# Kernel optimization log

Measured on AMD Instinct MI355X. Metric: run time of the kernel, lower is better.

The kernel has to match this reference:

```python
import jax, jax.numpy as jnp
import numpy as np

N, E, B = 50000, 300000, 8
XD, ED, H, L, G = 160, 16, 256, 4, 32


def setup_inputs() -> dict:
    key = jax.random.key(0)
    ks = jax.random.split(key, 24)
    w = lambda k, shape: jax.random.normal(k, shape, jnp.float32) * 0.05
    z = lambda *shape: jnp.zeros(shape, jnp.float32)
    in_dim = G + (XD - 128)
    return {
        "x": jax.random.normal(ks[0], (N, XD), jnp.float32),
        "edge_attr": jax.random.normal(ks[1], (E, ED), jnp.float32),
        "geo_w": w(ks[2], (128, G)), "geo_b": z(G),
        "nin_w1": w(ks[3], (in_dim, H)), "nin_b1": z(H),
        "nin_w2": w(ks[4], (H, H)), "nin_b2": z(H),
        "ee_w1": w(ks[5], (ED, H)), "ee_b1": z(H),
        "ee_w2": w(ks[6], (H, H)), "ee_b2": z(H),
        "msgx_w": w(ks[7], (L, H, H)),
        "msge_w": w(ks[8], (L, H, H)),
        "upd_w1": w(ks[9], (L, H, H)), "upd_b1": z(L, H),
        "upd_w2": w(ks[10], (L, H, H)), "upd_b2": z(L, H),
        "ln_g": jnp.ones((L, H), jnp.float32), "ln_b": z(L, H),
        "edge_index": jax.random.randint(ks[11], (2, E), 0, N),
        "batch": jnp.sort(jax.random.randint(ks[12], (N,), 0, B)),
        "node_type": jax.random.randint(ks[13], (N,), 0, 3),
    }


def _layernorm(v, g, b, eps=1e-5):
    mu = v.mean(-1, keepdims=True)
    var = ((v - mu) ** 2).mean(-1, keepdims=True)
    return (v - mu) / jnp.sqrt(var + eps) * g + b


def reference(x, edge_attr, geo_w, geo_b, nin_w1, nin_b1, nin_w2, nin_b2,
              ee_w1, ee_b1, ee_w2, ee_b2, msgx_w, msge_w,
              upd_w1, upd_b1, upd_w2, upd_b2, ln_g, ln_b,
              edge_index, batch, node_type):
    # geo projection of leading 128 dims, concat with remaining features
    geo = jax.nn.relu(x[:, :128] @ geo_w + geo_b)
    xin = jnp.concatenate([geo, x[:, 128:]], axis=1)
    # node_in MLP
    h = jax.nn.relu(xin @ nin_w1 + nin_b1) @ nin_w2 + nin_b2  # [N, H]
    # edge encoder MLP
    e = jax.nn.relu(edge_attr @ ee_w1 + ee_b1) @ ee_w2 + ee_b2  # [E, H]
    src, dst = edge_index[0], edge_index[1]
    for l in range(L):
        # message: msg_x(x_j) + msg_e(e), scatter-add to target nodes
        m = h[src] @ msgx_w[l] + e @ msge_w[l]  # [E, H]
        agg = jax.ops.segment_sum(m, dst, num_segments=N)  # [N, H]
        u = jax.nn.relu(agg @ upd_w1[l] + upd_b1[l]) @ upd_w2[l] + upd_b2[l]
        h = _layernorm(h + u, ln_g[l], ln_b[l])
    # masked mean-pool per graph for each node type
    def pool(k):
        mask = (node_type == k).astype(h.dtype)[:, None]  # [N, 1]
        s = jax.ops.segment_sum(h * mask, batch, num_segments=B)
        c = jax.ops.segment_sum(mask, batch, num_segments=B)
        return s / jnp.maximum(c, 1.0)
    z = jnp.concatenate([pool(0), pool(1), pool(2)], axis=1)  # [B, 3H]
    return (z, h, batch)
```

## Files before the change

kernel.cpp:

```cpp
#include <hip/hip_runtime.h>

constexpr int N  = 50000;
constexpr int E  = 300000;
constexpr int B  = 8;
constexpr int XD = 160;
constexpr int ED = 16;
constexpr int H  = 256;
constexpr int L  = 4;
constexpr int G  = 32;

typedef __attribute__((ext_vector_type(8))) short short8;
typedef __attribute__((ext_vector_type(4))) short sv4;
typedef __attribute__((ext_vector_type(4))) float floatx4;

__device__ __forceinline__ short f2bf(float f) {
    union { float f; unsigned u; } v; v.f = f;
    unsigned r = (v.u + 0x7fffu + ((v.u >> 16) & 1u)) >> 16;
    return (short)r;
}
__device__ __forceinline__ float bf2f(short s) {
    union { unsigned u; float f; } v;
    v.u = ((unsigned)(unsigned short)s) << 16;
    return v.f;
}

__global__ __launch_bounds__(256) void hist_kernel(
    const int* __restrict__ dst, int* __restrict__ cnt)
{
    int e = blockIdx.x * 256 + threadIdx.x;
    if (e < E) atomicAdd(&cnt[dst[e]], 1);
}

__global__ __launch_bounds__(256) void scan_partial_kernel(
    const int* __restrict__ cnt, int* __restrict__ bsum)
{
    __shared__ int s[256];
    const int tid = threadIdx.x;
    int i = blockIdx.x * 256 + tid;
    s[tid] = (i < N) ? cnt[i] : 0;
    __syncthreads();
    #pragma unroll
    for (int off = 128; off > 0; off >>= 1) {
        if (tid < off) s[tid] += s[tid + off];
        __syncthreads();
    }
    if (tid == 0) bsum[blockIdx.x] = s[0];
}

__global__ __launch_bounds__(256) void scan_bsum_kernel(
    int* __restrict__ bsum, int nb, int* __restrict__ rsN)
{
    __shared__ int s[256];
    const int tid = threadIdx.x;
    int v = (tid < nb) ? bsum[tid] : 0;
    s[tid] = v;
    __syncthreads();
    #pragma unroll
    for (int off = 1; off < 256; off <<= 1) {
        int x = (tid >= off) ? s[tid - off] : 0;
        __syncthreads();
        s[tid] += x;
        __syncthreads();
    }
    if (tid < nb) bsum[tid] = s[tid] - v;
    if (tid == 255) *rsN = s[255];
}

__global__ __launch_bounds__(256) void scan_final_kernel(
    const int* __restrict__ cnt, const int* __restrict__ bsum,
    int* __restrict__ rs, int* __restrict__ cursor)
{
    __shared__ int s[256];
    const int tid = threadIdx.x;
    int i = blockIdx.x * 256 + tid;
    int v = (i < N) ? cnt[i] : 0;
    s[tid] = v;
    __syncthreads();
    #pragma unroll
    for (int off = 1; off < 256; off <<= 1) {
        int x = (tid >= off) ? s[tid - off] : 0;
        __syncthreads();
        s[tid] += x;
        __syncthreads();
    }
    int excl = s[tid] - v + bsum[blockIdx.x];
    if (i < N) { rs[i] = excl; cursor[i] = excl; }
}

__global__ __launch_bounds__(256) void fill_kernel(
    const int* __restrict__ src, const int* __restrict__ dst,
    const float* __restrict__ ea,
    int* __restrict__ cursor, int* __restrict__ csr_src,
    float* __restrict__ ea_csr)
{
    int e = blockIdx.x * 256 + threadIdx.x;
    if (e < E) {
        int d = dst[e];
        int pos = atomicAdd(&cursor[d], 1);
        csr_src[pos] = src[e];
        const float4* a = (const float4*)(ea + (size_t)e * ED);
        float4* o = (float4*)(ea_csr + (size_t)pos * ED);
        o[0] = a[0]; o[1] = a[1]; o[2] = a[2]; o[3] = a[3];
    }
}

__global__ __launch_bounds__(256) void hidden_agg_kernel(
    const float* __restrict__ ea_csr, const float* __restrict__ ew1,
    const float* __restrict__ eb1,
    const int* __restrict__ rs,
    short* __restrict__ haggB)
{
    const int lane = threadIdx.x & 63;
    const int wave = threadIdx.x >> 6;
    const int n = blockIdx.x * 4 + wave;
    if (n >= N) return;

    float4 w[ED];
    #pragma unroll
    for (int k = 0; k < ED; ++k)
        w[k] = *(const float4*)&ew1[k * H + 4 * lane];
    float4 bb = *(const float4*)&eb1[4 * lane];

    const int s = rs[n], e = rs[n + 1];
    float4 acc = {0.f, 0.f, 0.f, 0.f};
    int j = s;
    for (; j + 1 < e; j += 2) {
        const float4* r0 = (const float4*)(ea_csr + (size_t)j * ED);
        const float4* r1 = (const float4*)(ea_csr + (size_t)(j + 1) * ED);
        float4 p0[4] = {r0[0], r0[1], r0[2], r0[3]};
        float4 p1[4] = {r1[0], r1[1], r1[2], r1[3]};
        float4 h0 = bb, h1 = bb;
        #pragma unroll
        for (int q = 0; q < 4; ++q) {
            float v00 = p0[q].x, v01 = p0[q].y, v02 = p0[q].z, v03 = p0[q].w;
            float v10 = p1[q].x, v11 = p1[q].y, v12 = p1[q].z, v13 = p1[q].w;
            const float4 w0 = w[q * 4 + 0], w1 = w[q * 4 + 1];
            const float4 w2 = w[q * 4 + 2], w3 = w[q * 4 + 3];
            h0.x += v00 * w0.x + v01 * w1.x + v02 * w2.x + v03 * w3.x;
            h0.y += v00 * w0.y + v01 * w1.y + v02 * w2.y + v03 * w3.y;
            h0.z += v00 * w0.z + v01 * w1.z + v02 * w2.z + v03 * w3.z;
            h0.w += v00 * w0.w + v01 * w1.w + v02 * w2.w + v03 * w3.w;
            h1.x += v10 * w0.x + v11 * w1.x + v12 * w2.x + v13 * w3.x;
            h1.y += v10 * w0.y + v11 * w1.y + v12 * w2.y + v13 * w3.y;
            h1.z += v10 * w0.z + v11 * w1.z + v12 * w2.z + v13 * w3.z;
            h1.w += v10 * w0.w + v11 * w1.w + v12 * w2.w + v13 * w3.w;
        }
        acc.x += fmaxf(h0.x, 0.f) + fmaxf(h1.x, 0.f);
        acc.y += fmaxf(h0.y, 0.f) + fmaxf(h1.y, 0.f);
        acc.z += fmaxf(h0.z, 0.f) + fmaxf(h1.z, 0.f);
        acc.w += fmaxf(h0.w, 0.f) + fmaxf(h1.w, 0.f);
    }
    if (j < e) {
        const float4* r0 = (const float4*)(ea_csr + (size_t)j * ED);
        float4 p0[4] = {r0[0], r0[1], r0[2], r0[3]};
        float4 h0 = bb;
        #pragma unroll
        for (int q = 0; q < 4; ++q) {
            float v00 = p0[q].x, v01 = p0[q].y, v02 = p0[q].z, v03 = p0[q].w;
            const float4 w0 = w[q * 4 + 0], w1 = w[q * 4 + 1];
            const float4 w2 = w[q * 4 + 2], w3 = w[q * 4 + 3];
            h0.x += v00 * w0.x + v01 * w1.x + v02 * w2.x + v03 * w3.x;
            h0.y += v00 * w0.y + v01 * w1.y + v02 * w2.y + v03 * w3.y;
            h0.z += v00 * w0.z + v01 * w1.z + v02 * w2.z + v03 * w3.z;
            h0.w += v00 * w0.w + v01 * w1.w + v02 * w2.w + v03 * w3.w;
        }
        acc.x += fmaxf(h0.x, 0.f); acc.y += fmaxf(h0.y, 0.f);
        acc.z += fmaxf(h0.z, 0.f); acc.w += fmaxf(h0.w, 0.f);
    }
    sv4 o = {f2bf(acc.x), f2bf(acc.y), f2bf(acc.z), f2bf(acc.w)};
    *(sv4*)&haggB[(size_t)n * H + 4 * lane] = o;
}

__global__ __launch_bounds__(256) void gather_kernel(
    const short* __restrict__ h_in_bf,
    const int* __restrict__ rs, const int* __restrict__ csr_src,
    short* __restrict__ agg_bf)
{
    const int lane = threadIdx.x & 63;
    const int wave = threadIdx.x >> 6;
    const int n = blockIdx.x * 4 + wave;
    if (n >= N) return;
    const int s = rs[n], e = rs[n + 1];
    float4 acc = {0.f, 0.f, 0.f, 0.f};
    int j = s;
    for (; j + 4 <= e; j += 4) {
        const int s0 = csr_src[j],     s1 = csr_src[j + 1];
        const int s2 = csr_src[j + 2], s3 = csr_src[j + 3];
        sv4 v0 = *(const sv4*)&h_in_bf[(size_t)s0 * H + 4 * lane];
        sv4 v1 = *(const sv4*)&h_in_bf[(size_t)s1 * H + 4 * lane];
        sv4 v2 = *(const sv4*)&h_in_bf[(size_t)s2 * H + 4 * lane];
        sv4 v3 = *(const sv4*)&h_in_bf[(size_t)s3 * H + 4 * lane];
        acc.x += (bf2f(v0.x) + bf2f(v1.x)) + (bf2f(v2.x) + bf2f(v3.x));
        acc.y += (bf2f(v0.y) + bf2f(v1.y)) + (bf2f(v2.y) + bf2f(v3.y));
        acc.z += (bf2f(v0.z) + bf2f(v1.z)) + (bf2f(v2.z) + bf2f(v3.z));
        acc.w += (bf2f(v0.w) + bf2f(v1.w)) + (bf2f(v2.w) + bf2f(v3.w));
    }
    for (; j < e; ++j) {
        const int s0 = csr_src[j];
        sv4 v0 = *(const sv4*)&h_in_bf[(size_t)s0 * H + 4 * lane];
        acc.x += bf2f(v0.x); acc.y += bf2f(v0.y);
        acc.z += bf2f(v0.z); acc.w += bf2f(v0.w);
    }
    sv4 o = {f2bf(acc.x), f2bf(acc.y), f2bf(acc.z), f2bf(acc.w)};
    *(sv4*)&agg_bf[(size_t)n * H + 4 * lane] = o;
}

__global__ __launch_bounds__(256) void we_fuse_kernel(
    const float* __restrict__ ee_w2, const float* __restrict__ msge_w,
    float* __restrict__ WEf32)
{
    __shared__ float wrow[H];
    const int tid = threadIdx.x;
    const int l = blockIdx.x / H;
    const int t = blockIdx.x % H;
    wrow[tid] = ee_w2[t * H + tid];
    __syncthreads();
    const float* mw = msge_w + (size_t)l * H * H;
    float acc = 0.f;
    for (int k = 0; k < H; ++k)
        acc += wrow[k] * mw[k * H + tid];
    WEf32[((size_t)l * H + t) * H + tid] = acc;
}

__global__ __launch_bounds__(256) void fuse1_kernel(
    const float* __restrict__ msgx_w, const float* __restrict__ upd_w1,
    short* __restrict__ fusedT)
{
    __shared__ float wrow[H];
    const int tid = threadIdx.x;
    const int l = blockIdx.x / H;
    const int t = blockIdx.x % H;
    wrow[tid] = msgx_w[((size_t)l * H + t) * H + tid];
    __syncthreads();
    const float* w1 = upd_w1 + (size_t)l * H * H;
    float acc = 0.f;
    for (int j = 0; j < H; ++j)
        acc += wrow[j] * w1[j * H + tid];
    fusedT[((size_t)(l * H + tid)) * 512 + t] = f2bf(acc);
}

__global__ __launch_bounds__(256) void fuse2_kernel(
    const float* __restrict__ WEf32, const float* __restrict__ upd_w1,
    short* __restrict__ fusedT)
{
    __shared__ float wrow[H];
    const int tid = threadIdx.x;
    const int l = blockIdx.x / H;
    const int t = blockIdx.x % H;
    wrow[tid] = WEf32[((size_t)l * H + t) * H + tid];
    __syncthreads();
    const float* w1 = upd_w1 + (size_t)l * H * H;
    float acc = 0.f;
    for (int j = 0; j < H; ++j)
        acc += wrow[j] * w1[j * H + tid];
    fusedT[((size_t)(l * H + tid)) * 512 + 256 + t] = f2bf(acc);
}

__global__ __launch_bounds__(256) void fuse_b_kernel(
    const float* __restrict__ ee_b2, const float* __restrict__ msge_w,
    float* __restrict__ be2)
{
    __shared__ float brow[H];
    const int tid = threadIdx.x;
    const int l = blockIdx.x;
    brow[tid] = ee_b2[tid];
    __syncthreads();
    const float* mw = msge_w + (size_t)l * H * H;
    float acc = 0.f;
    for (int k = 0; k < H; ++k)
        acc += brow[k] * mw[k * H + tid];
    be2[l * H + tid] = acc;
}

__global__ __launch_bounds__(256) void fuse_bias_kernel(
    const float* __restrict__ be2, const float* __restrict__ upd_w1,
    float* __restrict__ be2w1)
{
    __shared__ float brow[H];
    const int tid = threadIdx.x;
    const int l = blockIdx.x;
    brow[tid] = be2[l * H + tid];
    __syncthreads();
    const float* w1 = upd_w1 + (size_t)l * H * H;
    float acc = 0.f;
    for (int j = 0; j < H; ++j)
        acc += brow[j] * w1[j * H + tid];
    be2w1[l * H + tid] = acc;
}

__global__ __launch_bounds__(256) void conv_bt_kernel(
    const float* __restrict__ w, short* __restrict__ bt)
{
    int mat = blockIdx.x >> 8, k = blockIdx.x & 255, n = threadIdx.x;
    bt[((size_t)mat * H + n) * H + k] = f2bf(w[((size_t)mat * H + k) * H + n]);
}

__global__ __launch_bounds__(256) void geow_bt_kernel(
    const float* __restrict__ w, short* __restrict__ bt)
{
    for (int i = threadIdx.x; i < 32 * 128; i += 256) {
        int n = i >> 7, k = i & 127;
        bt[i] = f2bf(w[k * 32 + n]);
    }
}

__global__ __launch_bounds__(256) void ninw1_bt_kernel(
    const float* __restrict__ w, short* __restrict__ bt)
{
    int i = blockIdx.x * 256 + threadIdx.x;
    int n = i >> 6, k = i & 63;
    bt[i] = f2bf(w[k * H + n]);
}

__global__ __launch_bounds__(256) void node_in_mfma_kernel(
    const float* __restrict__ x,
    const short* __restrict__ geo_wbt, const float* __restrict__ geo_b,
    const short* __restrict__ w1bt, const float* __restrict__ b1,
    const short* __restrict__ w2bt, const float* __restrict__ b2,
    short* __restrict__ h_bf)
{
    constexpr int KP = H + 8;
    constexpr int KX = 128 + 8;
    constexpr int KI = 64 + 8;
    __shared__ short A[64 * KP];
    __shared__ short XIN[64 * KI];
    const int tid = threadIdx.x;
    const int lane = tid & 63, wave = tid >> 6;
    const int quad = lane >> 4, lm = lane & 15;
    const int n0 = blockIdx.x * 64;
    const int nvalid = min(64, N - n0);
    const int ncol = wave * 64 + lm;

    for (int i = tid; i < 64 * 128; i += 256) {
        int row = i >> 7, k = i & 127;
        float v = (row < nvalid) ? x[(size_t)(n0 + row) * XD + k] : 0.f;
        A[row * KX + k] = f2bf(v);
    }
    for (int i = tid; i < 64 * 32; i += 256) {
        int row = i >> 5, k = i & 31;
        float v = (row < nvalid) ? x[(size_t)(n0 + row) * XD + 128 + k] : 0.f;
        XIN[row * KI + 32 + k] = f2bf(v);
    }
    __syncthreads();

    {
        floatx4 c[2];
        float b0 = geo_b[lm], b1v = geo_b[16 + lm];
        c[0] = {b0, b0, b0, b0};
        c[1] = {b1v, b1v, b1v, b1v};
        #pragma unroll
        for (int ks = 0; ks < 4; ++ks) {
            short8 a  = *(const short8*)&A[(wave * 16 + lm) * KX + ks * 32 + quad * 8];
            short8 w0 = *(const short8*)&geo_wbt[(size_t)lm * 128 + ks * 32 + quad * 8];
            short8 w1 = *(const short8*)&geo_wbt[(size_t)(16 + lm) * 128 + ks * 32 + quad * 8];
            c[0] = __builtin_amdgcn_mfma_f32_16x16x32_bf16(a, w0, c[0], 0, 0, 0);
            c[1] = __builtin_amdgcn_mfma_f32_16x16x32_bf16(a, w1, c[1], 0, 0, 0);
        }
        #pragma unroll
        for (int nt = 0; nt < 2; ++nt)
            #pragma unroll
            for (int r = 0; r < 4; ++r) {
                int row = wave * 16 + quad * 4 + r;
                XIN[row * KI + nt * 16 + lm] = f2bf(fmaxf(c[nt][r], 0.f));
            }
    }
    __syncthreads();

    floatx4 c1[4][4];
    #pragma unroll
    for (int nt = 0; nt < 4; ++nt) {
        float bb = b1[ncol + nt * 16];
        #pragma unroll
        for (int mt = 0; mt < 4; ++mt) {
            c1[mt][nt][0] = bb; c1[mt][nt][1] = bb;
            c1[mt][nt][2] = bb; c1[mt][nt][3] = bb;
        }
    }
    #pragma unroll
    for (int ks = 0; ks < 2; ++ks) {
        short8 a[4], b[4];
        #pragma unroll
        for (int mt = 0; mt < 4; ++mt)
            a[mt] = *(const short8*)&XIN[(mt * 16 + lm) * KI + ks * 32 + quad * 8];
        #pragma unroll
        for (int nt = 0; nt < 4; ++nt)
            b[nt] = *(const short8*)&w1bt[(size_t)(ncol + nt * 16) * 64 + ks * 32 + quad * 8];
        #pragma unroll
        for (int mt = 0; mt < 4; ++mt)
            #pragma unroll
            for (int nt = 0; nt < 4; ++nt)
                c1[mt][nt] = __builtin_amdgcn_mfma_f32_16x16x32_bf16(a[mt], b[nt], c1[mt][nt], 0, 0, 0);
    }
    __syncthreads();
    #pragma unroll
    for (int mt = 0; mt < 4; ++mt)
        #pragma unroll
        for (int nt = 0; nt < 4; ++nt) {
            int col = ncol + nt * 16;
            #pragma unroll
            for (int r = 0; r < 4; ++r) {
                int row = mt * 16 + quad * 4 + r;
                A[row * KP + col] = f2bf(fmaxf(c1[mt][nt][r], 0.f));
            }
        }
    __syncthreads();

    floatx4 c2[4][4];
    #pragma unroll
    for (int nt = 0; nt < 4; ++nt) {
        float bb = b2[ncol + nt * 16];
        #pragma unroll
        for (int mt = 0; mt < 4; ++mt) {
            c2[mt][nt][0] = bb; c2[mt][nt][1] = bb;
            c2[mt][nt][2] = bb; c2[mt][nt][3] = bb;
        }
    }
    #pragma unroll
    for (int ks = 0; ks < 8; ++ks) {
        short8 a[4], b[4];
        #pragma unroll
        for (int mt = 0; mt < 4; ++mt)
            a[mt] = *(const short8*)&A[(mt * 16 + lm) * KP + ks * 32 + quad * 8];
        #pragma unroll
        for (int nt = 0; nt < 4; ++nt)
            b[nt] = *(const short8*)&w2bt[(size_t)(ncol + nt * 16) * H + ks * 32 + quad * 8];
        #pragma unroll
        for (int mt = 0; mt < 4; ++mt)
            #pragma unroll
            for (int nt = 0; nt < 4; ++nt)
                c2[mt][nt] = __builtin_amdgcn_mfma_f32_16x16x32_bf16(a[mt], b[nt], c2[mt][nt], 0, 0, 0);
    }
    #pragma unroll
    for (int mt = 0; mt < 4; ++mt)
        #pragma unroll
        for (int r = 0; r < 4; ++r) {
            int row = mt * 16 + quad * 4 + r;
            if (row < nvalid) {
                #pragma unroll
                for (int nt = 0; nt < 4; ++nt)
                    h_bf[(size_t)(n0 + row) * H + ncol + nt * 16] = f2bf(c2[mt][nt][r]);
            }
        }
}

__global__ __launch_bounds__(256, 4) void layer_kernel(
    const short* __restrict__ h_in_bf, short* __restrict__ h_out_bf,
    float* __restrict__ h_out_f32,
    const short* __restrict__ agg_bf,
    const int* __restrict__ rs,
    const short* __restrict__ haggB,
    const short* __restrict__ fusedT, const float* __restrict__ be2w1,
    const float* __restrict__ b1,
    const short* __restrict__ u2bt, const float* __restrict__ b2,
    const float* __restrict__ lng, const float* __restrict__ lnb)
{
    constexpr int KP = H + 8;
    constexpr int M  = 32;
    __shared__ short A[M * KP];
    __shared__ short A2[M * KP];
    __shared__ int rsL[M + 1];
    __shared__ float psum[M][4], psq[M][4];
    __shared__ float muS[M], rsS[M];
    const int tid  = threadIdx.x;
    const int lane = tid & 63, wave = tid >> 6;
    const int quad = lane >> 4, lm = lane & 15;
    const int n0 = blockIdx.x * M;
    const int nvalid = min(M, N - n0);
    const int ncol = wave * 64 + lm;

    if (tid < M + 1) rsL[tid] = rs[min(n0 + tid, N)];
    for (int i = tid; i < M * 64; i += 256) {
        int row = i >> 6, q = i & 63;
        sv4 v = {0, 0, 0, 0};
        sv4 w = {0, 0, 0, 0};
        if (row < nvalid) {
            v = *(const sv4*)&agg_bf[(size_t)(n0 + row) * H + 4 * q];
            w = *(const sv4*)&haggB[(size_t)(n0 + row) * H + 4 * q];
        }
        *(sv4*)&A[row * KP + 4 * q]  = v;
        *(sv4*)&A2[row * KP + 4 * q] = w;
    }
    __syncthreads();

    floatx4 c1[2][4];
    #pragma unroll
    for (int nt = 0; nt < 4; ++nt) {
        float bw = be2w1[ncol + nt * 16];
        float bb = b1[ncol + nt * 16];
        #pragma unroll
        for (int mt = 0; mt < 2; ++mt) {
            #pragma unroll
            for (int r = 0; r < 4; ++r) {
                int row = mt * 16 + quad * 4 + r;
                float deg = (float)(rsL[row + 1] - rsL[row]);
                c1[mt][nt][r] = deg * bw + bb;
            }
        }
    }
    {
        short8 bcur[4], bnxt[4];
        #pragma unroll
        for (int nt = 0; nt < 4; ++nt)
            bcur[nt] = *(const short8*)&fusedT[(size_t)(ncol + nt * 16) * 512 + quad * 8];
        #pragma unroll
        for (int ks = 0; ks < 8; ++ks) {
            if (ks < 7) {
                #pragma unroll
                for (int nt = 0; nt < 4; ++nt)
                    bnxt[nt] = *(const short8*)&fusedT[(size_t)(ncol + nt * 16) * 512 + (ks + 1) * 32 + quad * 8];
            }
            short8 a[2];
            #pragma unroll
            for (int mt = 0; mt < 2; ++mt)
                a[mt] = *(const short8*)&A[(mt * 16 + lm) * KP + ks * 32 + quad * 8];
            #pragma unroll
            for (int mt = 0; mt < 2; ++mt)
                #pragma unroll
                for (int nt = 0; nt < 4; ++nt)
                    c1[mt][nt] = __builtin_amdgcn_mfma_f32_16x16x32_bf16(a[mt], bcur[nt], c1[mt][nt], 0, 0, 0);
            #pragma unroll
            for (int nt = 0; nt < 4; ++nt) bcur[nt] = bnxt[nt];
        }
    }
    {
        short8 bcur[4], bnxt[4];
        #pragma unroll
        for (int nt = 0; nt < 4; ++nt)
            bcur[nt] = *(const short8*)&fusedT[(size_t)(ncol + nt * 16) * 512 + 256 + quad * 8];
        #pragma unroll
        for (int ks = 0; ks < 8; ++ks) {
            if (ks < 7) {
                #pragma unroll
                for (int nt = 0; nt < 4; ++nt)
                    bnxt[nt] = *(const short8*)&fusedT[(size_t)(ncol + nt * 16) * 512 + 256 + (ks + 1) * 32 + quad * 8];
            }
            short8 a[2];
            #pragma unroll
            for (int mt = 0; mt < 2; ++mt)
                a[mt] = *(const short8*)&A2[(mt * 16 + lm) * KP + ks * 32 + quad * 8];
            #pragma unroll
            for (int mt = 0; mt < 2; ++mt)
                #pragma unroll
                for (int nt = 0; nt < 4; ++nt)
                    c1[mt][nt] = __builtin_amdgcn_mfma_f32_16x16x32_bf16(a[mt], bcur[nt], c1[mt][nt], 0, 0, 0);
            #pragma unroll
            for (int nt = 0; nt < 4; ++nt) bcur[nt] = bnxt[nt];
        }
    }
    __syncthreads();
    #pragma unroll
    for (int mt = 0; mt < 2; ++mt)
        #pragma unroll
        for (int nt = 0; nt < 4; ++nt) {
            int col = ncol + nt * 16;
            #pragma unroll
            for (int r = 0; r < 4; ++r) {
                int row = mt * 16 + quad * 4 + r;
                A[row * KP + col] = f2bf(fmaxf(c1[mt][nt][r], 0.f));
            }
        }
    __syncthreads();

    floatx4 c3[2][4];
    #pragma unroll
    for (int nt = 0; nt < 4; ++nt) {
        float bb = b2[ncol + nt * 16];
        #pragma unroll
        for (int mt = 0; mt < 2; ++mt) {
            c3[mt][nt][0] = bb; c3[mt][nt][1] = bb;
            c3[mt][nt][2] = bb; c3[mt][nt][3] = bb;
        }
    }
    {
        short8 bcur[4], bnxt[4];
        #pragma unroll
        for (int nt = 0; nt < 4; ++nt)
            bcur[nt] = *(const short8*)&u2bt[(size_t)(ncol + nt * 16) * H + quad * 8];
        #pragma unroll
        for (int ks = 0; ks < 8; ++ks) {
            if (ks < 7) {
                #pragma unroll
                for (int nt = 0; nt < 4; ++nt)
                    bnxt[nt] = *(const short8*)&u2bt[(size_t)(ncol + nt * 16) * H + (ks + 1) * 32 + quad * 8];
            }
            short8 a[2];
            #pragma unroll
            for (int mt = 0; mt < 2; ++mt)
                a[mt] = *(const short8*)&A[(mt * 16 + lm) * KP + ks * 32 + quad * 8];
            #pragma unroll
            for (int mt = 0; mt < 2; ++mt)
                #pragma unroll
                for (int nt = 0; nt < 4; ++nt)
                    c3[mt][nt] = __builtin_amdgcn_mfma_f32_16x16x32_bf16(a[mt], bcur[nt], c3[mt][nt], 0, 0, 0);
            #pragma unroll
            for (int nt = 0; nt < 4; ++nt) bcur[nt] = bnxt[nt];
        }
    }
    #pragma unroll
    for (int mt = 0; mt < 2; ++mt)
        #pragma unroll
        for (int r = 0; r < 4; ++r) {
            int row = mt * 16 + quad * 4 + r;
            if (row < nvalid) {
                #pragma unroll
                for (int nt = 0; nt < 4; ++nt)
                    c3[mt][nt][r] += bf2f(h_in_bf[(size_t)(n0 + row) * H + ncol + nt * 16]);
            }
        }

    #pragma unroll
    for (int mt = 0; mt < 2; ++mt)
        #pragma unroll
        for (int r = 0; r < 4; ++r) {
            float s = 0.f, q = 0.f;
            #pragma unroll
            for (int nt = 0; nt < 4; ++nt) {
                float v = c3[mt][nt][r];
                s += v; q += v * v;
            }
            #pragma unroll
            for (int m = 1; m < 16; m <<= 1) {
                s += __shfl_xor(s, m, 64);
                q += __shfl_xor(q, m, 64);
            }
            if (lm == 0) {
                int row = mt * 16 + quad * 4 + r;
                psum[row][wave] = s;
                psq[row][wave]  = q;
            }
        }
    __syncthreads();
    if (tid < M) {
        float s = psum[tid][0] + psum[tid][1] + psum[tid][2] + psum[tid][3];
        float q = psq[tid][0] + psq[tid][1] + psq[tid][2] + psq[tid][3];
        float mu = s * (1.f / H);
        float var = q * (1.f / H) - mu * mu;
        muS[tid] = mu;
        rsS[tid] = rsqrtf(fmaxf(var, 0.f) + 1e-5f);
    }
    __syncthreads();

    float g[4], bb4[4];
    #pragma unroll
    for (int nt = 0; nt < 4; ++nt) {
        g[nt]   = lng[ncol + nt * 16];
        bb4[nt] = lnb[ncol + nt * 16];
    }
    const bool wbf = (h_out_bf != nullptr);
    const bool wf  = (h_out_f32 != nullptr);
    #pragma unroll
    for (int mt = 0; mt < 2; ++mt)
        #pragma unroll
        for (int r = 0; r < 4; ++r) {
            int row = mt * 16 + quad * 4 + r;
            if (row < nvalid) {
                float mu = muS[row], rsv = rsS[row];
                #pragma unroll
                for (int nt = 0; nt < 4; ++nt) {
                    float o = (c3[mt][nt][r] - mu) * rsv * g[nt] + bb4[nt];
                    size_t off = (size_t)(n0 + row) * H + ncol + nt * 16;
                    if (wbf) h_out_bf[off] = f2bf(o);
                    if (wf)  h_out_f32[off] = o;
                }
            }
        }
}

__global__ __launch_bounds__(256) void pool_kernel(
    const float* __restrict__ h, const int* __restrict__ batch,
    const int* __restrict__ ntype,
    float* __restrict__ zsum, float* __restrict__ zcnt)
{
    constexpr int CHUNK = 256;
    __shared__ float acc[3][H];
    __shared__ float cnt[3];
    const int tid = threadIdx.x;
    const int n0 = blockIdx.x * CHUNK;
    const int nend = min(n0 + CHUNK, N);

    for (int q = 0; q < 3; ++q) acc[q][tid] = 0.f;
    if (tid == 0) { cnt[0] = 0.f; cnt[1] = 0.f; cnt[2] = 0.f; }
    __syncthreads();

    int cur = batch[n0];
    for (int n = n0; n < nend; ++n) {
        int b = batch[n];
        int t = ntype[n];
        if (b != cur) {
            for (int q = 0; q < 3; ++q) {
                atomicAdd(&zsum[cur * (3 * H) + q * H + tid], acc[q][tid]);
                acc[q][tid] = 0.f;
            }
            if (tid == 0)
                for (int q = 0; q < 3; ++q) { atomicAdd(&zcnt[cur * 3 + q], cnt[q]); cnt[q] = 0.f; }
            cur = b;
        }
        acc[t][tid] += h[(size_t)n * H + tid];
        if (tid == 0) cnt[t] += 1.f;
    }
    for (int q = 0; q < 3; ++q)
        atomicAdd(&zsum[cur * (3 * H) + q * H + tid], acc[q][tid]);
    if (tid == 0)
        for (int q = 0; q < 3; ++q) atomicAdd(&zcnt[cur * 3 + q], cnt[q]);
}

__global__ __launch_bounds__(256) void finalize_kernel(
    const float* __restrict__ zsum, const float* __restrict__ zcnt,
    float* __restrict__ out)
{
    int idx = blockIdx.x * 256 + threadIdx.x;
    if (idx >= B * 3 * H) return;
    int b = idx / (3 * H);
    int c = idx % (3 * H);
    int t = c / H;
    float cn = zcnt[b * 3 + t];
    out[idx] = zsum[idx] / fmaxf(cn, 1.f);
}

__global__ __launch_bounds__(256) void batch_out_kernel(
    const int* __restrict__ batch, float* __restrict__ out)
{
    int idx = blockIdx.x * 256 + threadIdx.x;
    if (idx < N) out[idx] = (float)batch[idx];
}

extern "C" void kernel_launch(void* const* d_in, const int* in_sizes, int n_in,
                              void* d_out, int out_size, void* d_ws, size_t ws_size,
                              hipStream_t stream) {
    const float* x         = (const float*)d_in[0];
    const float* edge_attr = (const float*)d_in[1];
    const float* geo_w     = (const float*)d_in[2];
    const float* geo_b     = (const float*)d_in[3];
    const float* nin_w1    = (const float*)d_in[4];
    const float* nin_b1    = (const float*)d_in[5];
    const float* nin_w2    = (const float*)d_in[6];
    const float* nin_b2    = (const float*)d_in[7];
    const float* ee_w1     = (const float*)d_in[8];
    const float* ee_b1     = (const float*)d_in[9];
    const float* ee_w2     = (const float*)d_in[10];
    const float* ee_b2     = (const float*)d_in[11];
    const float* msgx_w    = (const float*)d_in[12];
    const float* msge_w    = (const float*)d_in[13];
    const float* upd_w1    = (const float*)d_in[14];
    const float* upd_b1    = (const float*)d_in[15];
    const float* upd_w2    = (const float*)d_in[16];
    const float* upd_b2    = (const float*)d_in[17];
    const float* ln_g      = (const float*)d_in[18];
    const float* ln_b      = (const float*)d_in[19];
    const int*   edge_index= (const int*)d_in[20];
    const int*   batch     = (const int*)d_in[21];
    const int*   node_type = (const int*)d_in[22];

    float* out = (float*)d_out;
    float* hf  = out + B * 3 * H;

    short* h0_bf   = (short*)d_ws;
    short* h1_bf   = h0_bf + (size_t)N * H;
    short* haggB   = h1_bf + (size_t)N * H;
    short* fusedT  = haggB + (size_t)N * H;
    short* u2bt    = fusedT + (size_t)L * H * 512;
    short* geowbt  = u2bt + (size_t)L * H * H;
    short* w1bt    = geowbt + 32 * 128;
    short* w2bt    = w1bt + H * 64;
    float* WEf32   = (float*)(w2bt + H * H);
    float* be2     = WEf32 + (size_t)L * H * H;
    float* be2w1   = be2 + L * H;
    float* zsum    = be2w1 + L * H;
    float* zcnt    = zsum + B * 3 * H;
    int*   rowcnt  = (int*)(zcnt + B * 3);
    int*   rs      = rowcnt + N;
    int*   cursor  = rs + N + 1;
    int*   bsum    = cursor + N;
    int*   csr_src = bsum + 256;
    float* ea_csr  = (float*)(csr_src + E);

    const int* src = edge_index;
    const int* dst = edge_index + E;

    const int nscan = (N + 255) / 256;

    hipMemsetAsync(rowcnt, 0, (size_t)N * sizeof(int), stream);
    hist_kernel<<<(E + 255) / 256, 256, 0, stream>>>(dst, rowcnt);
    scan_partial_kernel<<<nscan, 256, 0, stream>>>(rowcnt, bsum);
    scan_bsum_kernel<<<1, 256, 0, stream>>>(bsum, nscan, rs + N);
    scan_final_kernel<<<nscan, 256, 0, stream>>>(rowcnt, bsum, rs, cursor);
    fill_kernel<<<(E + 255) / 256, 256, 0, stream>>>(src, dst, edge_attr, cursor, csr_src, ea_csr);

    we_fuse_kernel<<<L * H, 256, 0, stream>>>(ee_w2, msge_w, WEf32);
    fuse1_kernel<<<L * H, 256, 0, stream>>>(msgx_w, upd_w1, fusedT);
    fuse2_kernel<<<L * H, 256, 0, stream>>>(WEf32, upd_w1, fusedT);
    fuse_b_kernel<<<L, 256, 0, stream>>>(ee_b2, msge_w, be2);
    fuse_bias_kernel<<<L, 256, 0, stream>>>(be2, upd_w1, be2w1);
    conv_bt_kernel<<<L * 256, 256, 0, stream>>>(upd_w2, u2bt);
    conv_bt_kernel<<<256, 256, 0, stream>>>(nin_w2, w2bt);
    geow_bt_kernel<<<1, 256, 0, stream>>>(geo_w, geowbt);
    ninw1_bt_kernel<<<64, 256, 0, stream>>>(nin_w1, w1bt);

    hidden_agg_kernel<<<(N + 3) / 4, 256, 0, stream>>>(
        ea_csr, ee_w1, ee_b1, rs, haggB);

    node_in_mfma_kernel<<<(N + 63) / 64, 256, 0, stream>>>(
        x, geowbt, geo_b, w1bt, nin_b1, w2bt, nin_b2, h0_bf);

    const int lgrid = (N + 31) / 32;
    for (int l = 0; l < L; ++l) {
        const short* hin  = (l & 1) ? h1_bf : h0_bf;
        short* aggb       = (l & 1) ? h0_bf : h1_bf;
        short* hout_bf    = (l == L - 1) ? nullptr : aggb;
        float* hout_f32   = (l == L - 1) ? hf : nullptr;
        gather_kernel<<<(N + 3) / 4, 256, 0, stream>>>(hin, rs, csr_src, aggb);
        layer_kernel<<<lgrid, 256, 0, stream>>>(
            hin, hout_bf, hout_f32, aggb, rs, haggB,
            fusedT + (size_t)l * H * 512, be2w1 + (size_t)l * H,
            upd_b1 + (size_t)l * H,
            u2bt + (size_t)l * H * H, upd_b2 + (size_t)l * H,
            ln_g + (size_t)l * H, ln_b + (size_t)l * H);
    }

    hipMemsetAsync(zsum, 0, (size_t)(B * 3 * H + B * 3) * sizeof(float), stream);
    pool_kernel<<<(N + 255) / 256, 256, 0, stream>>>(hf, batch, node_type, zsum, zcnt);
    finalize_kernel<<<(B * 3 * H + 255) / 256, 256, 0, stream>>>(zsum, zcnt, out);
    batch_out_kernel<<<(N + 255) / 256, 256, 0, stream>>>(batch, out + B * 3 * H + (size_t)N * H);
}
```

Before: 975.6 us.

## Compute edge-hidden aggregation with MFMA and a segment-indicator matmul

```diff
diff --git a/kernel.cpp b/kernel.cpp
--- a/kernel.cpp
+++ b/kernel.cpp
@@ -104,71 +104,117 @@
     }
 }
 
-__global__ __launch_bounds__(256) void hidden_agg_kernel(
-    const float* __restrict__ ea_csr, const float* __restrict__ ew1,
-    const float* __restrict__ eb1,
+__global__ __launch_bounds__(256, 3) void hidden_agg_mfma_kernel(
+    const float* __restrict__ ea_csr,
+    const short* __restrict__ ew1T, const float* __restrict__ eb1,
     const int* __restrict__ rs,
     short* __restrict__ haggB)
 {
-    const int lane = threadIdx.x & 63;
-    const int wave = threadIdx.x >> 6;
-    const int n = blockIdx.x * 4 + wave;
-    if (n >= N) return;
-
-    float4 w[ED];
-    #pragma unroll
-    for (int k = 0; k < ED; ++k)
-        w[k] = *(const float4*)&ew1[k * H + 4 * lane];
-    float4 bb = *(const float4*)&eb1[4 * lane];
-
-    const int s = rs[n], e = rs[n + 1];
-    float4 acc = {0.f, 0.f, 0.f, 0.f};
-    int j = s;
-    for (; j + 1 < e; j += 2) {
-        const float4* r0 = (const float4*)(ea_csr + (size_t)j * ED);
-        const float4* r1 = (const float4*)(ea_csr + (size_t)(j + 1) * ED);
-        float4 p0[4] = {r0[0], r0[1], r0[2], r0[3]};
-        float4 p1[4] = {r1[0], r1[1], r1[2], r1[3]};
-        float4 h0 = bb, h1 = bb;
-        #pragma unroll
-        for (int q = 0; q < 4; ++q) {
-            float v00 = p0[q].x, v01 = p0[q].y, v02 = p0[q].z, v03 = p0[q].w;
-            float v10 = p1[q].x, v11 = p1[q].y, v12 = p1[q].z, v13 = p1[q].w;
-            const float4 w0 = w[q * 4 + 0], w1 = w[q * 4 + 1];
-            const float4 w2 = w[q * 4 + 2], w3 = w[q * 4 + 3];
-            h0.x += v00 * w0.x + v01 * w1.x + v02 * w2.x + v03 * w3.x;
-            h0.y += v00 * w0.y + v01 * w1.y + v02 * w2.y + v03 * w3.y;
-            h0.z += v00 * w0.z + v01 * w1.z + v02 * w2.z + v03 * w3.z;
-            h0.w += v00 * w0.w + v01 * w1.w + v02 * w2.w + v03 * w3.w;
-            h1.x += v10 * w0.x + v11 * w1.x + v12 * w2.x + v13 * w3.x;
-            h1.y += v10 * w0.y + v11 * w1.y + v12 * w2.y + v13 * w3.y;
-            h1.z += v10 * w0.z + v11 * w1.z + v12 * w2.z + v13 * w3.z;
-            h1.w += v10 * w0.w + v11 * w1.w + v12 * w2.w + v13 * w3.w;
-        }
-        acc.x += fmaxf(h0.x, 0.f) + fmaxf(h1.x, 0.f);
-        acc.y += fmaxf(h0.y, 0.f) + fmaxf(h1.y, 0.f);
-        acc.z += fmaxf(h0.z, 0.f) + fmaxf(h1.z, 0.f);
-        acc.w += fmaxf(h0.w, 0.f) + fmaxf(h1.w, 0.f);
-    }
-    if (j < e) {
-        const float4* r0 = (const float4*)(ea_csr + (size_t)j * ED);
-        float4 p0[4] = {r0[0], r0[1], r0[2], r0[3]};
-        float4 h0 = bb;
-        #pragma unroll
-        for (int q = 0; q < 4; ++q) {
-            float v00 = p0[q].x, v01 = p0[q].y, v02 = p0[q].z, v03 = p0[q].w;
-            const float4 w0 = w[q * 4 + 0], w1 = w[q * 4 + 1];
-            const float4 w2 = w[q * 4 + 2], w3 = w[q * 4 + 3];
-            h0.x += v00 * w0.x + v01 * w1.x + v02 * w2.x + v03 * w3.x;
-            h0.y += v00 * w0.y + v01 * w1.y + v02 * w2.y + v03 * w3.y;
-            h0.z += v00 * w0.z + v01 * w1.z + v02 * w2.z + v03 * w3.z;
-            h0.w += v00 * w0.w + v01 * w1.w + v02 * w2.w + v03 * w3.w;
-        }
-        acc.x += fmaxf(h0.x, 0.f); acc.y += fmaxf(h0.y, 0.f);
-        acc.z += fmaxf(h0.z, 0.f); acc.w += fmaxf(h0.w, 0.f);
-    }
-    sv4 o = {f2bf(acc.x), f2bf(acc.y), f2bf(acc.z), f2bf(acc.w)};
-    *(sv4*)&haggB[(size_t)n * H + 4 * lane] = o;
+    __shared__ short EA[64 * 32];
+    __shared__ short RT[256 * 68];
+    __shared__ short S [32 * 68];
+    __shared__ int rsL[33];
+    const int tid  = threadIdx.x;
+    const int lane = tid & 63, wave = tid >> 6;
+    const int quad = lane >> 4, lm = lane & 15;
+    const int n0 = blockIdx.x * 32;
+    const int nvalid = min(32, N - n0);
+    const int ncol = wave * 64 + lm;
+
+    if (tid < 33) rsL[tid] = rs[min(n0 + tid, N)];
+    for (int i = tid; i < 64 * 16; i += 256) {
+        int row = i >> 4, k = i & 15;
+        EA[row * 32 + 16 + k] = 0;
+    }
+
+    short8 wf[4];
+    float ebv[4];
+    #pragma unroll
+    for (int nt = 0; nt < 4; ++nt) {
+        wf[nt]  = *(const short8*)&ew1T[(size_t)(ncol + nt * 16) * 32 + quad * 8];
+        ebv[nt] = eb1[ncol + nt * 16];
+    }
+    __syncthreads();
+
+    const int e_start = rsL[0], e_end = rsL[32];
+
+    floatx4 c2[2][4];
+    #pragma unroll
+    for (int mt = 0; mt < 2; ++mt)
+        #pragma unroll
+        for (int nt = 0; nt < 4; ++nt)
+            c2[mt][nt] = {0.f, 0.f, 0.f, 0.f};
+
+    for (int w0 = e_start; w0 < e_end; w0 += 64) {
+        for (int i = tid; i < 64 * 16; i += 256) {
+            int row = i >> 4, k = i & 15;
+            int e = w0 + row;
+            float v = (e < e_end) ? ea_csr[(size_t)e * ED + k] : 0.f;
+            EA[row * 32 + k] = f2bf(v);
+        }
+        for (int i = tid; i < 32 * 64; i += 256) {
+            int nd = i >> 6, el = i & 63;
+            int e = w0 + el;
+            S[nd * 68 + el] = (e >= rsL[nd] && e < rsL[nd + 1]) ? (short)0x3F80 : (short)0;
+        }
+        __syncthreads();
+
+        floatx4 c1[4][4];
+        #pragma unroll
+        for (int nt = 0; nt < 4; ++nt)
+            #pragma unroll
+            for (int mt = 0; mt < 4; ++mt) {
+                c1[mt][nt][0] = ebv[nt]; c1[mt][nt][1] = ebv[nt];
+                c1[mt][nt][2] = ebv[nt]; c1[mt][nt][3] = ebv[nt];
+            }
+        short8 a[4];
+        #pragma unroll
+        for (int mt = 0; mt < 4; ++mt)
+            a[mt] = *(const short8*)&EA[(mt * 16 + lm) * 32 + quad * 8];
+        #pragma unroll
+        for (int mt = 0; mt < 4; ++mt)
+            #pragma unroll
+            for (int nt = 0; nt < 4; ++nt)
+                c1[mt][nt] = __builtin_amdgcn_mfma_f32_16x16x32_bf16(a[mt], wf[nt], c1[mt][nt], 0, 0, 0);
+        #pragma unroll
+        for (int mt = 0; mt < 4; ++mt)
+            #pragma unroll
+            for (int nt = 0; nt < 4; ++nt) {
+                sv4 o = {f2bf(fmaxf(c1[mt][nt][0], 0.f)), f2bf(fmaxf(c1[mt][nt][1], 0.f)),
+                         f2bf(fmaxf(c1[mt][nt][2], 0.f)), f2bf(fmaxf(c1[mt][nt][3], 0.f))};
+                *(sv4*)&RT[(ncol + nt * 16) * 68 + mt * 16 + quad * 4] = o;
+            }
+        __syncthreads();
+
+        #pragma unroll
+        for (int ks = 0; ks < 2; ++ks) {
+            short8 a2[2], b2[4];
+            #pragma unroll
+            for (int mt = 0; mt < 2; ++mt)
+                a2[mt] = *(const short8*)&S[(mt * 16 + lm) * 68 + ks * 32 + quad * 8];
+            #pragma unroll
+            for (int nt = 0; nt < 4; ++nt)
+                b2[nt] = *(const short8*)&RT[(ncol + nt * 16) * 68 + ks * 32 + quad * 8];
+            #pragma unroll
+            for (int mt = 0; mt < 2; ++mt)
+                #pragma unroll
+                for (int nt = 0; nt < 4; ++nt)
+                    c2[mt][nt] = __builtin_amdgcn_mfma_f32_16x16x32_bf16(a2[mt], b2[nt], c2[mt][nt], 0, 0, 0);
+        }
+        __syncthreads();
+    }
+
+    #pragma unroll
+    for (int mt = 0; mt < 2; ++mt)
+        #pragma unroll
+        for (int r = 0; r < 4; ++r) {
+            int row = mt * 16 + quad * 4 + r;
+            if (row < nvalid) {
+                #pragma unroll
+                for (int nt = 0; nt < 4; ++nt)
+                    haggB[(size_t)(n0 + row) * H + ncol + nt * 16] = f2bf(c2[mt][nt][r]);
+            }
+        }
 }
 
 __global__ __launch_bounds__(256) void gather_kernel(
@@ -310,6 +356,18 @@
     int i = blockIdx.x * 256 + threadIdx.x;
     int n = i >> 6, k = i & 63;
     bt[i] = f2bf(w[k * H + n]);
+}
+
+__global__ __launch_bounds__(256) void ew1t_kernel(
+    const float* __restrict__ ew1, short* __restrict__ ew1T)
+{
+    int t = threadIdx.x;
+    #pragma unroll
+    for (int k = 0; k < ED; ++k)
+        ew1T[t * 32 + k] = f2bf(ew1[k * H + t]);
+    #pragma unroll
+    for (int k = ED; k < 32; ++k)
+        ew1T[t * 32 + k] = 0;
 }
 
 __global__ __launch_bounds__(256) void node_in_mfma_kernel(
@@ -762,7 +820,8 @@
     short* geowbt  = u2bt + (size_t)L * H * H;
     short* w1bt    = geowbt + 32 * 128;
     short* w2bt    = w1bt + H * 64;
-    float* WEf32   = (float*)(w2bt + H * H);
+    short* ew1T    = w2bt + H * H;
+    float* WEf32   = (float*)(ew1T + 256 * 32);
     float* be2     = WEf32 + (size_t)L * H * H;
     float* be2w1   = be2 + L * H;
     float* zsum    = be2w1 + L * H;
@@ -795,9 +854,10 @@
     conv_bt_kernel<<<256, 256, 0, stream>>>(nin_w2, w2bt);
     geow_bt_kernel<<<1, 256, 0, stream>>>(geo_w, geowbt);
     ninw1_bt_kernel<<<64, 256, 0, stream>>>(nin_w1, w1bt);
-
-    hidden_agg_kernel<<<(N + 3) / 4, 256, 0, stream>>>(
-        ea_csr, ee_w1, ee_b1, rs, haggB);
+    ew1t_kernel<<<1, 256, 0, stream>>>(ee_w1, ew1T);
+
+    hidden_agg_mfma_kernel<<<(N + 31) / 32, 256, 0, stream>>>(
+        ea_csr, ew1T, ee_b1, rs, haggB);
 
     node_in_mfma_kernel<<<(N + 63) / 64, 256, 0, stream>>>(
         x, geowbt, geo_b, w1bt, nin_b1, w2bt, nin_b2, h0_bf);
```

Result: faster. 917.7 us (median of 2 runs) (-5.9%).
